# Optimization experiments

Measured on AMD Instinct MI355X. Metric: run time of the kernel, lower is better.

The kernel has to match this reference:

```python
import jax, jax.numpy as jnp
import numpy as np

WCD, WCOV, WQUAL = 1.0, 1e-4, 1e-4
BIG = 1e10  # penalty to exclude zero-rows from min/argmin


def _calus(x, y):
    # x: [B, N, 3], y: [B, M, 3]
    B, N, _ = x.shape
    M = y.shape[1]
    # _remove_zero_rows filters rows whose coordinate SUM is zero -> mask instead
    mx = x.sum(-1) != 0  # [B, N] valid x points
    my = y.sum(-1) != 0  # [B, M] valid y points
    dt = x.dtype
    # squared pairwise distances d[b, j, i] = ||x[b,i] - y[b,j]||^2  (expanded form)
    xn = jnp.sum(x * x, axis=-1)  # [B, N]
    yn = jnp.sum(y * y, axis=-1)  # [B, M]
    d = yn[:, :, None] + xn[:, None, :] - 2.0 * jnp.einsum('bmc,bnc->bmn', y, x)  # [B, M, N]
    # push invalid rows/cols out of every min
    d = d + jnp.where(mx, 0.0, BIG).astype(dt)[:, None, :] \
          + jnp.where(my, 0.0, BIG).astype(dt)[:, :, None]
    x_min = jnp.min(d, axis=1)     # [B, N] nearest-y distance per x point
    x_arg = jnp.argmin(d, axis=1)  # [B, N] index into y
    y_min = jnp.min(d, axis=2)     # [B, M] nearest-x distance per y point
    y_arg = jnp.argmin(d, axis=2)  # [B, M] index into x
    fmx, fmy = mx.astype(dt), my.astype(dt)
    nx, ny = fmx.sum(-1), fmy.sum(-1)  # valid counts per sample
    # chamfer = mean over x-points + mean over y-points (torch cat+sum)
    cd = jnp.sum(x_min * fmx, -1) / nx + jnp.sum(y_min * fmy, -1) / ny  # [B]
    # coverage: fraction of y indices hit by some valid x point (unique count)
    rows = jnp.arange(B)[:, None]
    hit_y = jnp.zeros((B, M), dt).at[rows, x_arg].max(fmx)
    cov = hit_y.sum(-1) / ny  # [B]
    # quality: fraction of x indices hit by some valid y point
    hit_x = jnp.zeros((B, N), dt).at[rows, y_arg].max(fmy)
    qual = hit_x.sum(-1) / nx  # [B]
    return cd.mean(), cov.mean(), qual.mean()


def setup_inputs() -> dict:
    key = jax.random.key(0)
    kx, ky = jax.random.split(key)
    B, N, M = 32, 2048, 2048
    x = jax.random.normal(kx, (B, N, 3), dtype=jnp.float32)
    y = jax.random.normal(ky, (B, M, 3), dtype=jnp.float32)
    return {"x": x, "y": y}


def reference(x, y):
    cd, cov, qual = _calus(x, y)
    val = WCD * cd - WCOV * cov - WQUAL * qual
    return (val, cd, cov, qual)
```

## Files before the change

kernel.cpp:

```cpp
#include <hip/hip_runtime.h>
#include <stdint.h>


#define BB 32
#define NP 2048
#define BIGF 1e10f

__global__ __launch_bounds__(256) void nn_fused_kernel(const float* __restrict__ x,
                                                       const float* __restrict__ y,
                                                       unsigned* __restrict__ hitmask,
                                                       float* __restrict__ sums,
                                                       float* __restrict__ cnts) {
  int bid = blockIdx.x;
  int side = bid >> 8;
  int b = (bid >> 3) & 31;
  int pc = bid & 7;

  __shared__ float4 qs[NP];
  __shared__ float pxn[256];
  __shared__ float pvalid[256];
  __shared__ float2 merged[4][256];
  __shared__ float red[8];

  const float* qraw = (side ? x : y) + b * NP * 3;
  for (int k = 0; k < 8; ++k) {
    int i = threadIdx.x + 256 * k;
    float q0 = qraw[3 * i], q1 = qraw[3 * i + 1], q2 = qraw[3 * i + 2];
    float s = q0 + q1 + q2;
    float qn = q0 * q0 + q1 * q1 + q2 * q2;
    if (s == 0.0f) qn += BIGF;
    qs[i] = make_float4(-2.0f * q0, -2.0f * q1, -2.0f * q2, qn);
  }

  int w = threadIdx.x >> 6;
  int lane = threadIdx.x & 63;

  const float* praw = (side ? y : x) + (b * NP + pc * 256) * 3;
  float p0[4], p1[4], p2[4];
  for (int k = 0; k < 4; ++k) {
    int pl = lane + 64 * k;
    p0[k] = praw[3 * pl];
    p1[k] = praw[3 * pl + 1];
    p2[k] = praw[3 * pl + 2];
    if (w == 0) {
      float s = p0[k] + p1[k] + p2[k];
      pxn[pl] = p0[k] * p0[k] + p1[k] * p1[k] + p2[k] * p2[k];
      pvalid[pl] = (s != 0.0f) ? 1.0f : 0.0f;
    }
  }
  __syncthreads();

  float best0 = 3.0e38f, best1 = 3.0e38f, best2 = 3.0e38f, best3 = 3.0e38f;
  int bj0 = 0, bj1 = 0, bj2 = 0, bj3 = 0;
  const float4* qq = &qs[w * 512];
#pragma unroll 8
  for (int j = 0; j < 512; ++j) {
    float4 q = qq[j];
    float d0 = fmaf(q.x, p0[0], fmaf(q.y, p1[0], fmaf(q.z, p2[0], q.w)));
    float d1 = fmaf(q.x, p0[1], fmaf(q.y, p1[1], fmaf(q.z, p2[1], q.w)));
    float d2 = fmaf(q.x, p0[2], fmaf(q.y, p1[2], fmaf(q.z, p2[2], q.w)));
    float d3 = fmaf(q.x, p0[3], fmaf(q.y, p1[3], fmaf(q.z, p2[3], q.w)));
    if (d0 < best0) { best0 = d0; bj0 = j; }
    if (d1 < best1) { best1 = d1; bj1 = j; }
    if (d2 < best2) { best2 = d2; bj2 = j; }
    if (d3 < best3) { best3 = d3; bj3 = j; }
  }
  int qoff = w * 512;
  merged[w][lane +   0] = make_float2(best0, __int_as_float(qoff + bj0));
  merged[w][lane +  64] = make_float2(best1, __int_as_float(qoff + bj1));
  merged[w][lane + 128] = make_float2(best2, __int_as_float(qoff + bj2));
  merged[w][lane + 192] = make_float2(best3, __int_as_float(qoff + bj3));
  __syncthreads();

  int t = threadIdx.x;
  float2 e0 = merged[0][t];
  float bd = e0.x;
  int bi = __float_as_int(e0.y);
  for (int ww = 1; ww < 4; ++ww) {
    float2 e = merged[ww][t];
    if (e.x < bd) { bd = e.x; bi = __float_as_int(e.y); }
  }

  float valid = pvalid[t];
  float pmin = bd + pxn[t];
  float contrib = valid * pmin;
  if (valid != 0.0f)
    atomicOr(&hitmask[(side * BB + b) * 64 + (bi >> 5)], 1u << (bi & 31));

  float cnt = valid;
  for (int o = 32; o > 0; o >>= 1) {
    contrib += __shfl_down(contrib, o, 64);
    cnt += __shfl_down(cnt, o, 64);
  }
  if (lane == 0) { red[w] = contrib; red[4 + w] = cnt; }
  __syncthreads();
  if (t == 0) {
    atomicAdd(&sums[side * BB + b], red[0] + red[1] + red[2] + red[3]);
    atomicAdd(&cnts[side * BB + b], red[4] + red[5] + red[6] + red[7]);
  }
}

__global__ __launch_bounds__(64) void assemble_kernel(const unsigned* __restrict__ hitmask,
                                                      const float* __restrict__ sums,
                                                      const float* __restrict__ cnts,
                                                      float* __restrict__ out) {
  int t = threadIdx.x;
  float cd = 0.f, cov = 0.f, qual = 0.f;
  if (t < BB) {
    float nx = cnts[t], ny = cnts[BB + t];
    int hy = 0, hx = 0;
    for (int i = 0; i < 64; ++i) hy += __popc(hitmask[t * 64 + i]);
    for (int i = 0; i < 64; ++i) hx += __popc(hitmask[(BB + t) * 64 + i]);
    cd = sums[t] / nx + sums[BB + t] / ny;
    cov = (float)hy / ny;
    qual = (float)hx / nx;
  }
  for (int o = 32; o > 0; o >>= 1) {
    cd += __shfl_down(cd, o, 64);
    cov += __shfl_down(cov, o, 64);
    qual += __shfl_down(qual, o, 64);
  }
  if (t == 0) {
    cd /= (float)BB; cov /= (float)BB; qual /= (float)BB;
    out[0] = cd - 1e-4f * cov - 1e-4f * qual;
    out[1] = cd;
    out[2] = cov;
    out[3] = qual;
  }
}

extern "C" void kernel_launch(void* const* d_in, const int* in_sizes, int n_in,
                              void* d_out, int out_size, void* d_ws, size_t ws_size,
                              hipStream_t stream) {
  const float* x = (const float*)d_in[0];
  const float* y = (const float*)d_in[1];
  float* out = (float*)d_out;
  char* ws = (char*)d_ws;

  unsigned* hitmask = (unsigned*)ws;
  float* sums = (float*)(ws + 16384);
  float* cnts = sums + 2 * BB;

  hipMemsetAsync(ws, 0, 16384 + 512, stream);
  nn_fused_kernel<<<2 * BB * 8, 256, 0, stream>>>(x, y, hitmask, sums, cnts);
  assemble_kernel<<<1, 64, 0, stream>>>(hitmask, sums, cnts, out);
}
```

Measured before the change: 103.0 us.

## Split query scan over 8 waves and fuse final assembly via last-block counter

Blocks grow to 512 threads so each of 8 waves scans 256 query points instead of 512, halving the serial inner loop per wave and raising wave-level parallelism within each block. The separate assemble kernel is removed: a global atomic counter identifies the last block, which reads the hitmask, sums and counts and writes the outputs, saving one launch. This adds a threadfence, per-wave global atomics and a larger shared-memory merge buffer, and the launch bounds request more occupancy, which may limit registers.

After: 143.7 us. 39.6% more time.

```diff
diff --git a/kernel.cpp b/kernel.cpp
--- a/kernel.cpp
+++ b/kernel.cpp
@@ -5,26 +5,31 @@
 #define BB 32
 #define NP 2048
 #define BIGF 1e10f
+#define NBLK 512
 
-__global__ __launch_bounds__(256) void nn_fused_kernel(const float* __restrict__ x,
-                                                       const float* __restrict__ y,
-                                                       unsigned* __restrict__ hitmask,
-                                                       float* __restrict__ sums,
-                                                       float* __restrict__ cnts) {
+typedef unsigned int u32;
+
+__global__ __launch_bounds__(512, 4) void nn_fused_kernel(
+    const float* __restrict__ x, const float* __restrict__ y,
+    u32* __restrict__ hitmask, float* __restrict__ sums,
+    float* __restrict__ cnts, u32* __restrict__ counter,
+    float* __restrict__ out) {
   int bid = blockIdx.x;
   int side = bid >> 8;
   int b = (bid >> 3) & 31;
   int pc = bid & 7;
 
   __shared__ float4 qs[NP];
+  __shared__ float2 merged[8][256];
   __shared__ float pxn[256];
   __shared__ float pvalid[256];
-  __shared__ float2 merged[4][256];
-  __shared__ float red[8];
+  __shared__ int isLast;
+  __shared__ float l_cd, l_cov, l_qual;
 
+  int tid = threadIdx.x;
   const float* qraw = (side ? x : y) + b * NP * 3;
-  for (int k = 0; k < 8; ++k) {
-    int i = threadIdx.x + 256 * k;
+  for (int k = 0; k < 4; ++k) {
+    int i = tid + 512 * k;
     float q0 = qraw[3 * i], q1 = qraw[3 * i + 1], q2 = qraw[3 * i + 2];
     float s = q0 + q1 + q2;
     float qn = q0 * q0 + q1 * q1 + q2 * q2;
@@ -32,9 +37,7 @@
     qs[i] = make_float4(-2.0f * q0, -2.0f * q1, -2.0f * q2, qn);
   }
 
-  int w = threadIdx.x >> 6;
-  int lane = threadIdx.x & 63;
-
+  int w = tid >> 6, lane = tid & 63;
   const float* praw = (side ? y : x) + (b * NP + pc * 256) * 3;
   float p0[4], p1[4], p2[4];
   for (int k = 0; k < 4; ++k) {
@@ -43,18 +46,18 @@
     p1[k] = praw[3 * pl + 1];
     p2[k] = praw[3 * pl + 2];
     if (w == 0) {
-      float s = p0[k] + p1[k] + p2[k];
       pxn[pl] = p0[k] * p0[k] + p1[k] * p1[k] + p2[k] * p2[k];
-      pvalid[pl] = (s != 0.0f) ? 1.0f : 0.0f;
+      pvalid[pl] = ((p0[k] + p1[k] + p2[k]) != 0.0f) ? 1.0f : 0.0f;
     }
   }
+  if (tid == 0) { l_cd = 0.f; l_cov = 0.f; l_qual = 0.f; }
   __syncthreads();
 
   float best0 = 3.0e38f, best1 = 3.0e38f, best2 = 3.0e38f, best3 = 3.0e38f;
   int bj0 = 0, bj1 = 0, bj2 = 0, bj3 = 0;
-  const float4* qq = &qs[w * 512];
+  const float4* qq = &qs[w * 256];
 #pragma unroll 8
-  for (int j = 0; j < 512; ++j) {
+  for (int j = 0; j < 256; ++j) {
     float4 q = qq[j];
     float d0 = fmaf(q.x, p0[0], fmaf(q.y, p1[0], fmaf(q.z, p2[0], q.w)));
     float d1 = fmaf(q.x, p0[1], fmaf(q.y, p1[1], fmaf(q.z, p2[1], q.w)));
@@ -65,63 +68,61 @@
     if (d2 < best2) { best2 = d2; bj2 = j; }
     if (d3 < best3) { best3 = d3; bj3 = j; }
   }
-  int qoff = w * 512;
+  int qoff = w * 256;
   merged[w][lane +   0] = make_float2(best0, __int_as_float(qoff + bj0));
   merged[w][lane +  64] = make_float2(best1, __int_as_float(qoff + bj1));
   merged[w][lane + 128] = make_float2(best2, __int_as_float(qoff + bj2));
   merged[w][lane + 192] = make_float2(best3, __int_as_float(qoff + bj3));
   __syncthreads();
 
-  int t = threadIdx.x;
-  float2 e0 = merged[0][t];
-  float bd = e0.x;
-  int bi = __float_as_int(e0.y);
-  for (int ww = 1; ww < 4; ++ww) {
-    float2 e = merged[ww][t];
-    if (e.x < bd) { bd = e.x; bi = __float_as_int(e.y); }
+  float contrib = 0.f, cnt = 0.f;
+  if (tid < 256) {
+    float2 e0 = merged[0][tid];
+    float bd = e0.x;
+    int bi = __float_as_int(e0.y);
+    for (int ww = 1; ww < 8; ++ww) {
+      float2 e = merged[ww][tid];
+      if (e.x < bd) { bd = e.x; bi = __float_as_int(e.y); }
+    }
+    float valid = pvalid[tid];
+    contrib = valid * (bd + pxn[tid]);
+    cnt = valid;
+    if (valid != 0.0f)
+      atomicOr(&hitmask[(side * BB + b) * 64 + (bi >> 5)], 1u << (bi & 31));
   }
-
-  float valid = pvalid[t];
-  float pmin = bd + pxn[t];
-  float contrib = valid * pmin;
-  if (valid != 0.0f)
-    atomicOr(&hitmask[(side * BB + b) * 64 + (bi >> 5)], 1u << (bi & 31));
-
-  float cnt = valid;
   for (int o = 32; o > 0; o >>= 1) {
     contrib += __shfl_down(contrib, o, 64);
     cnt += __shfl_down(cnt, o, 64);
   }
-  if (lane == 0) { red[w] = contrib; red[4 + w] = cnt; }
+  if (lane == 0 && w < 4) {
+    atomicAdd(&sums[side * BB + b], contrib);
+    atomicAdd(&cnts[side * BB + b], cnt);
+  }
+
+  __threadfence();
   __syncthreads();
-  if (t == 0) {
-    atomicAdd(&sums[side * BB + b], red[0] + red[1] + red[2] + red[3]);
-    atomicAdd(&cnts[side * BB + b], red[4] + red[5] + red[6] + red[7]);
+  if (tid == 0) isLast = (atomicAdd(counter, 1u) == NBLK - 1);
+  __syncthreads();
+  if (!isLast) return;
+
+  int sb = tid >> 3, c = tid & 7;
+  float h = 0.f;
+  for (int i = 0; i < 8; ++i)
+    h += (float)__popc(atomicOr(&hitmask[sb * 64 + c * 8 + i], 0u));
+  h += __shfl_down(h, 4, 8);
+  h += __shfl_down(h, 2, 8);
+  h += __shfl_down(h, 1, 8);
+  if (c == 0) {
+    float sv = atomicAdd(&sums[sb], 0.0f);
+    float cv = atomicAdd(&cnts[sb], 0.0f);
+    float ocv = atomicAdd(&cnts[sb ^ 32], 0.0f);
+    atomicAdd(&l_cd, sv / cv);
+    if (sb < 32) atomicAdd(&l_cov, h / ocv);
+    else         atomicAdd(&l_qual, h / ocv);
   }
-}
-
-__global__ __launch_bounds__(64) void assemble_kernel(const unsigned* __restrict__ hitmask,
-                                                      const float* __restrict__ sums,
-                                                      const float* __restrict__ cnts,
-                                                      float* __restrict__ out) {
-  int t = threadIdx.x;
-  float cd = 0.f, cov = 0.f, qual = 0.f;
-  if (t < BB) {
-    float nx = cnts[t], ny = cnts[BB + t];
-    int hy = 0, hx = 0;
-    for (int i = 0; i < 64; ++i) hy += __popc(hitmask[t * 64 + i]);
-    for (int i = 0; i < 64; ++i) hx += __popc(hitmask[(BB + t) * 64 + i]);
-    cd = sums[t] / nx + sums[BB + t] / ny;
-    cov = (float)hy / ny;
-    qual = (float)hx / nx;
-  }
-  for (int o = 32; o > 0; o >>= 1) {
-    cd += __shfl_down(cd, o, 64);
-    cov += __shfl_down(cov, o, 64);
-    qual += __shfl_down(qual, o, 64);
-  }
-  if (t == 0) {
-    cd /= (float)BB; cov /= (float)BB; qual /= (float)BB;
+  __syncthreads();
+  if (tid == 0) {
+    float cd = l_cd / (float)BB, cov = l_cov / (float)BB, qual = l_qual / (float)BB;
     out[0] = cd - 1e-4f * cov - 1e-4f * qual;
     out[1] = cd;
     out[2] = cov;
@@ -137,11 +138,11 @@
   float* out = (float*)d_out;
   char* ws = (char*)d_ws;
 
-  unsigned* hitmask = (unsigned*)ws;
+  u32* hitmask = (u32*)ws;
   float* sums = (float*)(ws + 16384);
   float* cnts = sums + 2 * BB;
+  u32* counter = (u32*)(cnts + 2 * BB);
 
-  hipMemsetAsync(ws, 0, 16384 + 512, stream);
-  nn_fused_kernel<<<2 * BB * 8, 256, 0, stream>>>(x, y, hitmask, sums, cnts);
-  assemble_kernel<<<1, 64, 0, stream>>>(hitmask, sums, cnts, out);
+  hipMemsetAsync(ws, 0, 16384 + 512 + 4, stream);
+  nn_fused_kernel<<<NBLK, 512, 0, stream>>>(x, y, hitmask, sums, cnts, counter, out);
 }
```
